# Kernel optimization log

Hardware: AMD Instinct MI355X
Metric: run time of the kernel (lower is better)

The kernel has to match this reference:

```python
import jax, jax.numpy as jnp
import numpy as np

N_NODES = 100_000
N_EDGES = 3_200_000
N_FEAT = 128
N_HID = 8
N_CLASSES = 10


def setup_inputs() -> dict:
    key = jax.random.key(0)
    ks = jax.random.split(key, 16)
    g = lambda k, shape, fan_in: jax.random.normal(k, shape, jnp.float32) / np.sqrt(fan_in)
    inp = {}
    inp['x'] = jax.random.normal(ks[0], (N_NODES, N_FEAT), jnp.float32)
    inp['edge_index'] = jax.random.randint(ks[1], (2, N_EDGES), 0, N_NODES, jnp.int32)
    # lin: Linear(F, 8)
    inp['lin_w'] = g(ks[2], (N_FEAT, N_HID), N_FEAT)
    inp['lin_b'] = jnp.zeros((N_HID,), jnp.float32)
    # conv1: GATConv(8, 8, heads=2)
    inp['w1'] = g(ks[3], (N_HID, 2 * N_HID), N_HID)
    inp['a1_src'] = g(ks[4], (2, N_HID), N_HID)
    inp['a1_dst'] = g(ks[5], (2, N_HID), N_HID)
    inp['b1'] = jnp.zeros((2 * N_HID,), jnp.float32)
    # conv2: GATConv(16, 8, heads=2)
    inp['w2'] = g(ks[6], (2 * N_HID, 2 * N_HID), 2 * N_HID)
    inp['a2_src'] = g(ks[7], (2, N_HID), N_HID)
    inp['a2_dst'] = g(ks[8], (2, N_HID), N_HID)
    inp['b2'] = jnp.zeros((2 * N_HID,), jnp.float32)
    # conv3: GATConv(16, num_classes, heads=1, concat=False)
    inp['w3'] = g(ks[9], (2 * N_HID, N_CLASSES), 2 * N_HID)
    inp['a3_src'] = g(ks[10], (1, N_CLASSES), N_CLASSES)
    inp['a3_dst'] = g(ks[11], (1, N_CLASSES), N_CLASSES)
    inp['b3'] = jnp.zeros((N_CLASSES,), jnp.float32)
    return inp


def _gat_conv(x, W, a_src, a_dst, b, src, dst, heads, out_c, concat):
    """PyG GATConv with pre-appended self-loops in (src, dst)."""
    N = x.shape[0]
    xl = (x @ W).reshape(N, heads, out_c)                 # [N,H,C]
    alpha_src = (xl * a_src[None]).sum(-1)                # [N,H]
    alpha_dst = (xl * a_dst[None]).sum(-1)                # [N,H]
    e = jax.nn.leaky_relu(alpha_src[src] + alpha_dst[dst], 0.2)  # [E,H]
    # segment softmax over destination nodes
    m = jax.ops.segment_max(e, dst, num_segments=N)
    e = jnp.exp(e - m[dst])
    s = jax.ops.segment_sum(e, dst, num_segments=N)
    alpha = e / s[dst]                                    # [E,H]
    msg = xl[src] * alpha[:, :, None]                     # [E,H,C]
    out = jax.ops.segment_sum(msg, dst, num_segments=N)   # [N,H,C]
    out = out.reshape(N, heads * out_c) if concat else out.mean(axis=1)
    return out + b


def reference(x, edge_index, lin_w, lin_b, w1, a1_src, a1_dst, b1,
              w2, a2_src, a2_dst, b2, w3, a3_src, a3_dst, b3):
    N = x.shape[0]
    loops = jnp.arange(N, dtype=edge_index.dtype)
    src = jnp.concatenate([edge_index[0], loops])
    dst = jnp.concatenate([edge_index[1], loops])
    lrelu = lambda v: jax.nn.leaky_relu(v, 0.01)
    h = lrelu(x @ lin_w + lin_b)
    h = lrelu(_gat_conv(h, w1, a1_src, a1_dst, b1, src, dst, 2, N_HID, True))
    h = lrelu(_gat_conv(h, w2, a2_src, a2_dst, b2, src, dst, 2, N_HID, True))
    h = _gat_conv(h, w3, a3_src, a3_dst, b3, src, dst, 1, N_CLASSES, False)
    return jax.nn.log_softmax(h, axis=-1)
```

## Files before the change

### kernel.cpp

```cpp
#include <hip/hip_runtime.h>
#include <hip/hip_fp16.h>
#include <math.h>

#define N_NODES 100000
#define N_EDGES 3200000
#define ET (N_EDGES + N_NODES)
#define SLOT 80
#define KMAX 5
#define SHIFT 8
#define BNODES 256
#define NBUCK 391
#define P1_T 1024
#define E_PER 8
#define P1_WG ((N_EDGES + P1_T * E_PER - 1) / (P1_T * E_PER))
#define BUILD_T 1024
#define SCAN_T 1024
#define SCAN_CHUNK 98
#define LOG2E 1.44269504088896f

typedef _Float16 h2 __attribute__((ext_vector_type(2)));

__device__ __forceinline__ float lrelu(float v, float s) { return v > 0.f ? v : v * s; }
__device__ __forceinline__ float fexp2(float x) { return __builtin_amdgcn_exp2f(x); }

__device__ __forceinline__ h2 f2h2(float f) {
    union { float f; h2 h; } u; u.f = f; return u.h;
}

__device__ __forceinline__ float fdot2(h2 a, h2 b, float c) {
#if __has_builtin(__builtin_amdgcn_fdot2)
    return __builtin_amdgcn_fdot2(a, b, c, false);
#else
    return c + (float)a.x * (float)b.x + (float)a.y * (float)b.y;
#endif
}

template <int CTRL>
__device__ __forceinline__ float dppmov(float v) {
    return __int_as_float(__builtin_amdgcn_update_dpp(0, __float_as_int(v), CTRL, 0xF, 0xF, true));
}

__device__ __forceinline__ void reduce8(float a[8], float& ssum, int lane) {
    int b0 = lane & 1, b1 = (lane >> 1) & 1, b2 = (lane >> 2) & 1;
    float q0 = (b0 ? a[4] : a[0]) + dppmov<0xB1>(b0 ? a[0] : a[4]);
    float q1 = (b0 ? a[5] : a[1]) + dppmov<0xB1>(b0 ? a[1] : a[5]);
    float q2 = (b0 ? a[6] : a[2]) + dppmov<0xB1>(b0 ? a[2] : a[6]);
    float q3 = (b0 ? a[7] : a[3]) + dppmov<0xB1>(b0 ? a[3] : a[7]);
    float r0 = (b1 ? q2 : q0) + dppmov<0x4E>(b1 ? q0 : q2);
    float r1 = (b1 ? q3 : q1) + dppmov<0x4E>(b1 ? q1 : q3);
    float t  = (b2 ? r1 : r0) + __shfl_xor(b2 ? r0 : r1, 4, 64);
    t += __shfl_xor(t, 8, 64);
    a[0] = t;
    ssum += dppmov<0xB1>(ssum);
    ssum += dppmov<0x4E>(ssum);
    ssum += __shfl_xor(ssum, 4, 64);
    ssum += __shfl_xor(ssum, 8, 64);
}

__global__ void __launch_bounds__(P1_T) part_kernel(const int* __restrict__ ei,
                                                    int* __restrict__ starts,
                                                    unsigned* __restrict__ pairs) {
    __shared__ int hist[NBUCK];
    __shared__ int scan[512];
    int t = threadIdx.x;
    for (int i = t; i < NBUCK; i += P1_T) hist[i] = 0;
    __syncthreads();
    int base = blockIdx.x * (P1_T * E_PER);
    int s[E_PER], d[E_PER], r[E_PER];
#pragma unroll
    for (int k = 0; k < E_PER; k++) {
        int e = base + k * P1_T + t;
        if (e < N_EDGES) {
            s[k] = ei[e];
            d[k] = ei[N_EDGES + e];
            r[k] = atomicAdd(&hist[d[k] >> SHIFT], 1);
        }
    }
    __syncthreads();
    if (t < 512) scan[t] = (t < NBUCK) ? hist[t] : 0;
    __syncthreads();
    for (int off = 1; off < 512; off <<= 1) {
        int v = 0, add = 0;
        if (t < 512) { v = scan[t]; if (t >= off) add = scan[t - off]; }
        __syncthreads();
        if (t < 512) scan[t] = v + add;
        __syncthreads();
    }
    if (t <= NBUCK) starts[blockIdx.x * (NBUCK + 1) + t] = base + (t ? scan[t - 1] : 0);
#pragma unroll
    for (int k = 0; k < E_PER; k++) {
        int e = base + k * P1_T + t;
        if (e < N_EDGES) {
            int b = d[k] >> SHIFT;
            int pos = (b ? scan[b - 1] : 0) + r[k];
            pairs[base + pos] = ((unsigned)(d[k] & (BNODES - 1)) << 17) | (unsigned)s[k];
        }
    }
}

__global__ void __launch_bounds__(BUILD_T) build_kernel(const int* __restrict__ starts,
                                                        const unsigned* __restrict__ pairs,
                                                        int* __restrict__ csr,
                                                        int* __restrict__ deg) {
    __shared__ int offs[BNODES];
    int b = blockIdx.x;
    int t = threadIdx.x;
    int node0 = b << SHIFT;
    if (t < BNODES) {
        int n = node0 + t;
        if (n < N_NODES) {
            csr[n * SLOT] = n;
            offs[t] = 1;
        } else offs[t] = 0;
    }
    __syncthreads();
    int wid = t >> 6, lane = t & 63;
    for (int B = wid; B < P1_WG; B += (BUILD_T / 64)) {
        int st = starts[B * (NBUCK + 1) + b];
        int en = starts[B * (NBUCK + 1) + b + 1];
        for (int i = st + lane; i < en; i += 64) {
            unsigned v = pairs[i];
            int ln = v >> 17;
            int sc = v & 0x1FFFF;
            int pos = atomicAdd(&offs[ln], 1);
            if (pos < SLOT) csr[(node0 + ln) * SLOT + pos] = sc;
        }
    }
    __syncthreads();
    if (t < BNODES) {
        int n = node0 + t;
        if (n < N_NODES) deg[n] = offs[t];
    }
}

__global__ void count_kernel(const int* __restrict__ ei, int* __restrict__ deg) {
    int e = blockIdx.x * blockDim.x + threadIdx.x;
    if (e >= ET) return;
    int d = (e < N_EDGES) ? ei[N_EDGES + e] : (e - N_EDGES);
    atomicAdd(&deg[d], 1);
}

__global__ void scan_kernel(const int* __restrict__ deg, int* __restrict__ rowptr,
                            int* __restrict__ cursor) {
    __shared__ int sums[SCAN_T];
    int t = threadIdx.x;
    int start = t * SCAN_CHUNK;
    int end = min(start + SCAN_CHUNK, N_NODES);
    int s = 0;
    for (int i = start; i < end; i++) s += deg[i];
    sums[t] = s;
    __syncthreads();
    for (int off = 1; off < SCAN_T; off <<= 1) {
        int v = sums[t];
        int add = (t >= off) ? sums[t - off] : 0;
        __syncthreads();
        sums[t] = v + add;
        __syncthreads();
    }
    int base = (t > 0) ? sums[t - 1] : 0;
    for (int i = start; i < end; i++) {
        rowptr[i] = base;
        cursor[i] = base;
        base += deg[i];
    }
    if (t == SCAN_T - 1) rowptr[N_NODES] = base;
}

__global__ void scatter_kernel(const int* __restrict__ ei, int* __restrict__ cursor,
                               int* __restrict__ csr) {
    int e = blockIdx.x * blockDim.x + threadIdx.x;
    if (e >= ET) return;
    int s, d;
    if (e < N_EDGES) { s = ei[e]; d = ei[N_EDGES + e]; } else { s = d = e - N_EDGES; }
    int pos = atomicAdd(&cursor[d], 1);
    csr[pos] = s;
}

template <int CIN, int H, int C, int XLS>
__global__ void prep_kernel(const float* __restrict__ hin, const float* __restrict__ W,
                            const float* __restrict__ a_src, const float* __restrict__ a_dst,
                            __half* __restrict__ xl, float* __restrict__ asrc,
                            float* __restrict__ adst) {
    __shared__ float Ws[CIN * H * C];
    __shared__ float As[H * C];
    __shared__ float Ad[H * C];
    for (int i = threadIdx.x; i < CIN * H * C; i += blockDim.x) Ws[i] = W[i];
    for (int i = threadIdx.x; i < H * C; i += blockDim.x) {
        As[i] = a_src[i] * LOG2E;
        Ad[i] = a_dst[i] * LOG2E;
    }
    __syncthreads();
    int n = blockIdx.x * blockDim.x + threadIdx.x;
    if (n >= N_NODES) return;
    float hreg[CIN];
#pragma unroll
    for (int i = 0; i < CIN; i += 4) {
        float4 v = *(const float4*)&hin[n * CIN + i];
        hreg[i] = v.x; hreg[i + 1] = v.y; hreg[i + 2] = v.z; hreg[i + 3] = v.w;
    }
#pragma unroll
    for (int h = 0; h < H; h++) {
        float as = 0.f, ad = 0.f;
#pragma unroll
        for (int c = 0; c < C; c++) {
            float v = 0.f;
#pragma unroll
            for (int i = 0; i < CIN; i++) v += hreg[i] * Ws[i * H * C + h * C + c];
            xl[n * XLS + h * C + c] = __float2half_rn(v);
            as += v * As[h * C + c];
            ad += v * Ad[h * C + c];
        }
        asrc[n * H + h] = as;
        adst[n * H + h] = ad;
    }
#pragma unroll
    for (int c = H * C; c < XLS; c++) xl[n * XLS + c] = __float2half_rn(0.f);
}

template <int H, int C, int XLS>
__global__ __launch_bounds__(256) void prep_lin_kernel(
        const float* __restrict__ x, const float* __restrict__ lw, const float* __restrict__ lb,
        const float* __restrict__ W, const float* __restrict__ a_src,
        const float* __restrict__ a_dst, __half* __restrict__ xl,
        float* __restrict__ asrc, float* __restrict__ adst) {
    __shared__ float LW[128 * 8];
    __shared__ float Ws[8 * H * C];
    __shared__ float As[H * C];
    __shared__ float Ad[H * C];
    __shared__ float Lb[8];
    for (int i = threadIdx.x; i < 128 * 8; i += 256) LW[i] = lw[i];
    for (int i = threadIdx.x; i < 8 * H * C; i += 256) Ws[i] = W[i];
    for (int i = threadIdx.x; i < H * C; i += 256) {
        As[i] = a_src[i] * LOG2E;
        Ad[i] = a_dst[i] * LOG2E;
    }
    if (threadIdx.x < 8) Lb[threadIdx.x] = lb[threadIdx.x];
    __syncthreads();
    int n = blockIdx.x * blockDim.x + threadIdx.x;
    if (n >= N_NODES) return;
    float hreg[8];
#pragma unroll
    for (int c = 0; c < 8; c++) hreg[c] = 0.f;
#pragma unroll 8
    for (int i = 0; i < 128; i += 4) {
        float4 v = *(const float4*)&x[n * 128 + i];
#pragma unroll
        for (int c = 0; c < 8; c++) hreg[c] += v.x * LW[(i + 0) * 8 + c];
#pragma unroll
        for (int c = 0; c < 8; c++) hreg[c] += v.y * LW[(i + 1) * 8 + c];
#pragma unroll
        for (int c = 0; c < 8; c++) hreg[c] += v.z * LW[(i + 2) * 8 + c];
#pragma unroll
        for (int c = 0; c < 8; c++) hreg[c] += v.w * LW[(i + 3) * 8 + c];
    }
#pragma unroll
    for (int c = 0; c < 8; c++) hreg[c] = lrelu(hreg[c] + Lb[c], 0.01f);
#pragma unroll
    for (int h = 0; h < H; h++) {
        float as = 0.f, ad = 0.f;
#pragma unroll
        for (int c = 0; c < C; c++) {
            float v = 0.f;
#pragma unroll
            for (int i = 0; i < 8; i++) v += hreg[i] * Ws[i * H * C + h * C + c];
            xl[n * XLS + h * C + c] = __float2half_rn(v);
            as += v * As[h * C + c];
            ad += v * Ad[h * C + c];
        }
        asrc[n * H + h] = as;
        adst[n * H + h] = ad;
    }
#pragma unroll
    for (int c = H * C; c < XLS; c++) xl[n * XLS + c] = __float2half_rn(0.f);
}

__global__ __launch_bounds__(256) void gat64_h2(const int* __restrict__ cnt_,
                                                const int* __restrict__ csr,
                                                const float* __restrict__ a_src,
                                                const float* __restrict__ adst,
                                                const __half* __restrict__ xl,
                                                const float* __restrict__ b,
                                                float* __restrict__ hout) {
    int wg = blockIdx.x * 4 + (threadIdx.x >> 6);
    int lane = threadIdx.x & 63;
    int eg = lane & 15;
    int q  = (lane >> 4) & 1;
    int nd = lane >> 5;
    int n = wg * 2 + nd;
    float4 as0 = *(const float4*)&a_src[q * 8];
    float4 as1 = *(const float4*)&a_src[q * 8 + 4];
    h2 av0 = {(_Float16)(as0.x * LOG2E), (_Float16)(as0.y * LOG2E)};
    h2 av1 = {(_Float16)(as0.z * LOG2E), (_Float16)(as0.w * LOG2E)};
    h2 av2 = {(_Float16)(as1.x * LOG2E), (_Float16)(as1.y * LOG2E)};
    h2 av3 = {(_Float16)(as1.z * LOG2E), (_Float16)(as1.w * LOG2E)};
    int cnt = min(cnt_[n], SLOT);
    float ad = adst[n * 2 + q];
    int idx[KMAX];
#pragma unroll
    for (int k = 0; k < KMAX; k++) {
        int i = eg + (k << 4);
        idx[k] = (i < cnt) ? csr[n * SLOT + i] : -1;
    }
    float ssum = 0.f;
    float a[8] = {0.f, 0.f, 0.f, 0.f, 0.f, 0.f, 0.f, 0.f};
#pragma unroll
    for (int k = 0; k < KMAX; k++) {
        int s = idx[k];
        if (s >= 0) {
            float4 raw = *(const float4*)&xl[s * 16 + q * 8];
            h2 x0 = f2h2(raw.x), x1 = f2h2(raw.y), x2 = f2h2(raw.z), x3 = f2h2(raw.w);
            float e = fdot2(x0, av0, fdot2(x1, av1, fdot2(x2, av2, fdot2(x3, av3, ad))));
            float w = fexp2(fmaxf(e, 0.2f * e));
            ssum += w;
            a[0] += w * (float)x0.x; a[1] += w * (float)x0.y;
            a[2] += w * (float)x1.x; a[3] += w * (float)x1.y;
            a[4] += w * (float)x2.x; a[5] += w * (float)x2.y;
            a[6] += w * (float)x3.x; a[7] += w * (float)x3.y;
        }
    }
    reduce8(a, ssum, lane);
    if ((lane & 8) == 0) {
        int ch = 8 * q + 4 * (lane & 1) + 2 * ((lane >> 1) & 1) + ((lane >> 2) & 1);
        hout[n * 16 + ch] = lrelu(a[0] / ssum + b[ch], 0.01f);
    }
}

__global__ __launch_bounds__(256) void gat64_ls(const int* __restrict__ cnt_,
                                                const int* __restrict__ csr,
                                                const float* __restrict__ a_src,
                                                const float* __restrict__ adst,
                                                const __half* __restrict__ xl,
                                                const float* __restrict__ b,
                                                float* __restrict__ out) {
    int wg = blockIdx.x * 4 + (threadIdx.x >> 6);
    int lane = threadIdx.x & 63;
    int eg = lane & 15;
    int q  = (lane >> 4) & 1;
    int nd = lane >> 5;
    int n = wg * 2 + nd;
    float avf[8];
#pragma unroll
    for (int j = 0; j < 8; j++) {
        int c = q * 8 + j;
        avf[j] = (c < 10) ? a_src[c] * LOG2E : 0.f;
    }
    h2 av0 = {(_Float16)avf[0], (_Float16)avf[1]};
    h2 av1 = {(_Float16)avf[2], (_Float16)avf[3]};
    h2 av2 = {(_Float16)avf[4], (_Float16)avf[5]};
    h2 av3 = {(_Float16)avf[6], (_Float16)avf[7]};
    int cnt = min(cnt_[n], SLOT);
    float adh = adst[n] * 0.5f;
    int idx[KMAX];
#pragma unroll
    for (int k = 0; k < KMAX; k++) {
        int i = eg + (k << 4);
        idx[k] = (i < cnt) ? csr[n * SLOT + i] : -1;
    }
    float ssum = 0.f;
    float a[8] = {0.f, 0.f, 0.f, 0.f, 0.f, 0.f, 0.f, 0.f};
#pragma unroll
    for (int k = 0; k < KMAX; k++) {
        int s = idx[k];
        if (s >= 0) {
            float4 raw = *(const float4*)&xl[s * 16 + q * 8];
            h2 x0 = f2h2(raw.x), x1 = f2h2(raw.y), x2 = f2h2(raw.z), x3 = f2h2(raw.w);
            float part = fdot2(x0, av0, fdot2(x1, av1, fdot2(x2, av2, fdot2(x3, av3, adh))));
            float e = part + __shfl_xor(part, 16, 64);
            float w = fexp2(fmaxf(e, 0.2f * e));
            ssum += w;
            a[0] += w * (float)x0.x; a[1] += w * (float)x0.y;
            a[2] += w * (float)x1.x; a[3] += w * (float)x1.y;
            a[4] += w * (float)x2.x; a[5] += w * (float)x2.y;
            a[6] += w * (float)x3.x; a[7] += w * (float)x3.y;
        }
    }
    reduce8(a, ssum, lane);
    int ch = 8 * q + 4 * (lane & 1) + 2 * ((lane >> 1) & 1) + ((lane >> 2) & 1);
    float u = (ch < 10) ? a[0] / ssum + b[ch] : -INFINITY;
    float m = u;
    m = fmaxf(m, dppmov<0xB1>(m));
    m = fmaxf(m, dppmov<0x4E>(m));
    m = fmaxf(m, __shfl_xor(m, 4, 64));
    m = fmaxf(m, __shfl_xor(m, 8, 64));
    m = fmaxf(m, __shfl_xor(m, 16, 64));
    float ex = (ch < 10 && (lane & 8) == 0) ? __expf(u - m) : 0.f;
    ex += dppmov<0xB1>(ex);
    ex += dppmov<0x4E>(ex);
    ex += __shfl_xor(ex, 4, 64);
    ex += __shfl_xor(ex, 8, 64);
    ex += __shfl_xor(ex, 16, 64);
    float lse = m + __logf(ex);
    if ((lane & 8) == 0 && ch < 10) out[n * 10 + ch] = u - lse;
}

__global__ void gat16_h2(const int* __restrict__ rowptr, const int* __restrict__ csr,
                         const float* __restrict__ asrc, const float* __restrict__ adst,
                         const __half* __restrict__ xl, const float* __restrict__ b,
                         float* __restrict__ hout) {
    int tid = blockIdx.x * blockDim.x + threadIdx.x;
    int wave = tid >> 6;
    int lane = threadIdx.x & 63;
    int g = lane >> 4;
    int c = lane & 15;
    int h = c >> 3;
    int n = wave * 4 + g;
    if (n >= N_NODES) return;
    int beg = rowptr[n], cnt = rowptr[n + 1] - beg;
    float adn = adst[n * 2 + h];
    float ssum = 0.f, pa = 0.f;
#pragma unroll 4
    for (int i = 0; i < cnt; i++) {
        int s = csr[beg + i];
        float e = asrc[s * 2 + h] + adn;
        float w = fexp2(fmaxf(e, 0.2f * e));
        ssum += w;
        pa += w * __half2float(xl[s * 16 + c]);
    }
    hout[n * 16 + c] = lrelu(pa / ssum + b[c], 0.01f);
}

__global__ void gat16_ls(const int* __restrict__ rowptr, const int* __restrict__ csr,
                         const float* __restrict__ asrc, const float* __restrict__ adst,
                         const __half* __restrict__ xl, const float* __restrict__ b,
                         float* __restrict__ out) {
    int tid = blockIdx.x * blockDim.x + threadIdx.x;
    int wave = tid >> 6;
    int lane = threadIdx.x & 63;
    int g = lane >> 4;
    int c = lane & 15;
    int n = wave * 4 + g;
    if (n >= N_NODES) return;
    int beg = rowptr[n], cnt = rowptr[n + 1] - beg;
    float adn = adst[n];
    float ssum = 0.f, pa = 0.f;
#pragma unroll 4
    for (int i = 0; i < cnt; i++) {
        int s = csr[beg + i];
        float e = asrc[s] + adn;
        float w = fexp2(fmaxf(e, 0.2f * e));
        ssum += w;
        pa += w * __half2float(xl[s * 16 + c]);
    }
    float v = pa / ssum + ((c < 10) ? b[c] : 0.f);
    float vm = (c < 10) ? v : -INFINITY;
#pragma unroll
    for (int off = 8; off >= 1; off >>= 1) vm = fmaxf(vm, __shfl_xor(vm, off, 16));
    float ex = (c < 10) ? __expf(v - vm) : 0.f;
    float sum = ex;
#pragma unroll
    for (int off = 8; off >= 1; off >>= 1) sum += __shfl_xor(sum, off, 16);
    float lse = vm + __logf(sum);
    if (c < 10) out[n * 10 + c] = v - lse;
}

extern "C" void kernel_launch(void* const* d_in, const int* in_sizes, int n_in,
                              void* d_out, int out_size, void* d_ws, size_t ws_size,
                              hipStream_t stream) {
    const float* x     = (const float*)d_in[0];
    const int*   ei    = (const int*)d_in[1];
    const float* lin_w = (const float*)d_in[2];
    const float* lin_b = (const float*)d_in[3];
    const float* w1    = (const float*)d_in[4];
    const float* a1s   = (const float*)d_in[5];
    const float* a1d   = (const float*)d_in[6];
    const float* b1    = (const float*)d_in[7];
    const float* w2    = (const float*)d_in[8];
    const float* a2s   = (const float*)d_in[9];
    const float* a2d   = (const float*)d_in[10];
    const float* b2    = (const float*)d_in[11];
    const float* w3    = (const float*)d_in[12];
    const float* a3s   = (const float*)d_in[13];
    const float* a3d   = (const float*)d_in[14];
    const float* b3    = (const float*)d_in[15];

    float* ws = (float*)d_ws;
    float* slotH  = ws;
    __half* slotX = (__half*)(ws + 1600000);
    float* as_    = ws + 3200000;
    float* ad_    = ws + 3400000;
    unsigned* pairs = (unsigned*)ws;
    int* csrP = (int*)(ws + 3600000);
    int* degP = csrP + (size_t)N_NODES * SLOT;
    int* startsP = degP + N_NODES;
    size_t need_new = (size_t)(3600000 + (size_t)N_NODES * SLOT + N_NODES
                               + (size_t)P1_WG * (NBUCK + 1) + 64) * 4;

    int use_bucket = (ws_size >= need_new) ? 1 : 0;

    int* degC    = (int*)(ws + 3600000);
    int* rowptrC = degC + N_NODES;
    int* cursorC = rowptrC + N_NODES + 1;
    int* csrC    = cursorC + N_NODES;

    dim3 B(256);
    int nb_n  = (N_NODES + 255) / 256;
    int nb_et = (ET + 255) / 256;
    int nb_g  = (N_NODES + 15) / 16;
    int nb_w2 = N_NODES / 8;

    if (use_bucket) {
        part_kernel<<<P1_WG, P1_T, 0, stream>>>(ei, startsP, pairs);
        build_kernel<<<NBUCK, BUILD_T, 0, stream>>>(startsP, pairs, csrP, degP);
    } else {
        hipMemsetAsync(degC, 0, N_NODES * sizeof(int), stream);
        count_kernel<<<nb_et, B, 0, stream>>>(ei, degC);
        scan_kernel<<<1, SCAN_T, 0, stream>>>(degC, rowptrC, cursorC);
        scatter_kernel<<<nb_et, B, 0, stream>>>(ei, cursorC, csrC);
    }

    prep_lin_kernel<2, 8, 16><<<nb_n, B, 0, stream>>>(x, lin_w, lin_b, w1, a1s, a1d,
                                                      slotX, as_, ad_);
    if (use_bucket) gat64_h2<<<nb_w2, B, 0, stream>>>(degP, csrP, a1s, ad_, slotX, b1, slotH);
    else            gat16_h2<<<nb_g, B, 0, stream>>>(rowptrC, csrC, as_, ad_, slotX, b1, slotH);

    prep_kernel<16, 2, 8, 16><<<nb_n, B, 0, stream>>>(slotH, w2, a2s, a2d, slotX, as_, ad_);
    if (use_bucket) gat64_h2<<<nb_w2, B, 0, stream>>>(degP, csrP, a2s, ad_, slotX, b2, slotH);
    else            gat16_h2<<<nb_g, B, 0, stream>>>(rowptrC, csrC, as_, ad_, slotX, b2, slotH);

    prep_kernel<16, 1, 10, 16><<<nb_n, B, 0, stream>>>(slotH, w3, a3s, a3d, slotX, as_, ad_);
    if (use_bucket) gat64_ls<<<nb_w2, B, 0, stream>>>(degP, csrP, a3s, ad_, slotX, b3, (float*)d_out);
    else            gat16_ls<<<nb_g, B, 0, stream>>>(rowptrC, csrC, as_, ad_, slotX, b3, (float*)d_out);
}
```

Before: 280.2 us.

## Fuse linear prep into partition kernel and next-layer prep into GAT aggregation

Result: faster. 274.0 us (-2.2%).

```diff
diff --git a/kernel.cpp b/kernel.cpp
--- a/kernel.cpp
+++ b/kernel.cpp
@@ -13,6 +13,7 @@
 #define P1_T 1024
 #define E_PER 8
 #define P1_WG ((N_EDGES + P1_T * E_PER - 1) / (P1_T * E_PER))
+#define NB_N ((N_NODES + 255) / 256)
 #define BUILD_T 1024
 #define SCAN_T 1024
 #define SCAN_CHUNK 98
@@ -57,43 +58,90 @@
     ssum += __shfl_xor(ssum, 8, 64);
 }
 
-__global__ void __launch_bounds__(P1_T) part_kernel(const int* __restrict__ ei,
-                                                    int* __restrict__ starts,
-                                                    unsigned* __restrict__ pairs) {
+__global__ void __launch_bounds__(P1_T) partlin_kernel(
+        const int* __restrict__ ei, int* __restrict__ starts, unsigned* __restrict__ pairs,
+        const float* __restrict__ x, const float* __restrict__ lw, const float* __restrict__ lb,
+        const float* __restrict__ W, const float* __restrict__ a_dst,
+        __half* __restrict__ xl, float* __restrict__ adst) {
     __shared__ int hist[NBUCK];
     __shared__ int scan[512];
+    __shared__ float LW[128 * 8];
+    __shared__ float Ws[8 * 16];
+    __shared__ float Ad[16];
+    __shared__ float Lb[8];
     int t = threadIdx.x;
-    for (int i = t; i < NBUCK; i += P1_T) hist[i] = 0;
-    __syncthreads();
-    int base = blockIdx.x * (P1_T * E_PER);
-    int s[E_PER], d[E_PER], r[E_PER];
-#pragma unroll
-    for (int k = 0; k < E_PER; k++) {
-        int e = base + k * P1_T + t;
-        if (e < N_EDGES) {
-            s[k] = ei[e];
-            d[k] = ei[N_EDGES + e];
-            r[k] = atomicAdd(&hist[d[k] >> SHIFT], 1);
-        }
-    }
-    __syncthreads();
-    if (t < 512) scan[t] = (t < NBUCK) ? hist[t] : 0;
-    __syncthreads();
-    for (int off = 1; off < 512; off <<= 1) {
-        int v = 0, add = 0;
-        if (t < 512) { v = scan[t]; if (t >= off) add = scan[t - off]; }
+    if (blockIdx.x < P1_WG) {
+        for (int i = t; i < NBUCK; i += P1_T) hist[i] = 0;
         __syncthreads();
-        if (t < 512) scan[t] = v + add;
+        int base = blockIdx.x * (P1_T * E_PER);
+        int s[E_PER], d[E_PER], r[E_PER];
+#pragma unroll
+        for (int k = 0; k < E_PER; k++) {
+            int e = base + k * P1_T + t;
+            if (e < N_EDGES) {
+                s[k] = ei[e];
+                d[k] = ei[N_EDGES + e];
+                r[k] = atomicAdd(&hist[d[k] >> SHIFT], 1);
+            }
+        }
         __syncthreads();
-    }
-    if (t <= NBUCK) starts[blockIdx.x * (NBUCK + 1) + t] = base + (t ? scan[t - 1] : 0);
-#pragma unroll
-    for (int k = 0; k < E_PER; k++) {
-        int e = base + k * P1_T + t;
-        if (e < N_EDGES) {
-            int b = d[k] >> SHIFT;
-            int pos = (b ? scan[b - 1] : 0) + r[k];
-            pairs[base + pos] = ((unsigned)(d[k] & (BNODES - 1)) << 17) | (unsigned)s[k];
+        if (t < 512) scan[t] = (t < NBUCK) ? hist[t] : 0;
+        __syncthreads();
+        for (int off = 1; off < 512; off <<= 1) {
+            int v = 0, add = 0;
+            if (t < 512) { v = scan[t]; if (t >= off) add = scan[t - off]; }
+            __syncthreads();
+            if (t < 512) scan[t] = v + add;
+            __syncthreads();
+        }
+        if (t <= NBUCK) starts[blockIdx.x * (NBUCK + 1) + t] = base + (t ? scan[t - 1] : 0);
+#pragma unroll
+        for (int k = 0; k < E_PER; k++) {
+            int e = base + k * P1_T + t;
+            if (e < N_EDGES) {
+                int b = d[k] >> SHIFT;
+                int pos = (b ? scan[b - 1] : 0) + r[k];
+                pairs[base + pos] = ((unsigned)(d[k] & (BNODES - 1)) << 17) | (unsigned)s[k];
+            }
+        }
+    } else {
+        for (int i = t; i < 128 * 8; i += P1_T) LW[i] = lw[i];
+        for (int i = t; i < 8 * 16; i += P1_T) Ws[i] = W[i];
+        for (int i = t; i < 16; i += P1_T) Ad[i] = a_dst[i] * LOG2E;
+        if (t < 8) Lb[t] = lb[t];
+        __syncthreads();
+        if (t >= 256) return;
+        int n = (blockIdx.x - P1_WG) * 256 + t;
+        if (n >= N_NODES) return;
+        float hreg[8];
+#pragma unroll
+        for (int c = 0; c < 8; c++) hreg[c] = 0.f;
+#pragma unroll 8
+        for (int i = 0; i < 128; i += 4) {
+            float4 v = *(const float4*)&x[n * 128 + i];
+#pragma unroll
+            for (int c = 0; c < 8; c++) hreg[c] += v.x * LW[(i + 0) * 8 + c];
+#pragma unroll
+            for (int c = 0; c < 8; c++) hreg[c] += v.y * LW[(i + 1) * 8 + c];
+#pragma unroll
+            for (int c = 0; c < 8; c++) hreg[c] += v.z * LW[(i + 2) * 8 + c];
+#pragma unroll
+            for (int c = 0; c < 8; c++) hreg[c] += v.w * LW[(i + 3) * 8 + c];
+        }
+#pragma unroll
+        for (int c = 0; c < 8; c++) hreg[c] = lrelu(hreg[c] + Lb[c], 0.01f);
+#pragma unroll
+        for (int h = 0; h < 2; h++) {
+            float ad = 0.f;
+#pragma unroll
+            for (int c = 0; c < 8; c++) {
+                float v = 0.f;
+#pragma unroll
+                for (int i = 0; i < 8; i++) v += hreg[i] * Ws[i * 16 + h * 8 + c];
+                xl[n * 16 + h * 8 + c] = __float2half_rn(v);
+                ad += v * Ad[h * 8 + c];
+            }
+            adst[n * 2 + h] = ad;
         }
     }
 }
@@ -274,14 +322,22 @@
     for (int c = H * C; c < XLS; c++) xl[n * XLS + c] = __float2half_rn(0.f);
 }
 
-__global__ __launch_bounds__(256) void gat64_h2(const int* __restrict__ cnt_,
-                                                const int* __restrict__ csr,
-                                                const float* __restrict__ a_src,
-                                                const float* __restrict__ adst,
-                                                const __half* __restrict__ xl,
-                                                const float* __restrict__ b,
-                                                float* __restrict__ hout) {
-    int wg = blockIdx.x * 4 + (threadIdx.x >> 6);
+template <int CN, int HN>
+__global__ __launch_bounds__(256) void gat64_h2_fused(
+        const int* __restrict__ cnt_, const int* __restrict__ csr,
+        const float* __restrict__ a_src, const float* __restrict__ adst,
+        const __half* __restrict__ xl, const float* __restrict__ b,
+        const float* __restrict__ Wn_g, const float* __restrict__ adn_g,
+        __half* __restrict__ xl_next, float* __restrict__ adst_next) {
+    __shared__ float hsm[8][16];
+    __shared__ float vsm[8][16];
+    __shared__ float Wn[16 * CN];
+    __shared__ float Adn[CN];
+    for (int i = threadIdx.x; i < 16 * CN; i += 256) Wn[i] = Wn_g[i];
+    for (int i = threadIdx.x; i < CN; i += 256) Adn[i] = adn_g[i] * LOG2E;
+
+    int wid = threadIdx.x >> 6;
+    int wg = blockIdx.x * 4 + wid;
     int lane = threadIdx.x & 63;
     int eg = lane & 15;
     int q  = (lane >> 4) & 1;
@@ -321,7 +377,28 @@
     reduce8(a, ssum, lane);
     if ((lane & 8) == 0) {
         int ch = 8 * q + 4 * (lane & 1) + 2 * ((lane >> 1) & 1) + ((lane >> 2) & 1);
-        hout[n * 16 + ch] = lrelu(a[0] / ssum + b[ch], 0.01f);
+        hsm[(wid << 1) | nd][ch] = lrelu(a[0] / ssum + b[ch], 0.01f);
+    }
+    __syncthreads();
+    if (threadIdx.x < 128) {
+        int ln = threadIdx.x >> 4, c = threadIdx.x & 15;
+        float v = 0.f;
+        if (c < CN) {
+#pragma unroll
+            for (int i = 0; i < 16; i++) v += hsm[ln][i] * Wn[i * CN + c];
+        }
+        int n2 = blockIdx.x * 8 + ln;
+        xl_next[n2 * 16 + c] = __float2half_rn(v);
+        vsm[ln][c] = v;
+    }
+    __syncthreads();
+    if (threadIdx.x < 8 * HN) {
+        int ln = threadIdx.x / HN, h = threadIdx.x % HN;
+        const int CH = CN / HN;
+        float adn = 0.f;
+#pragma unroll
+        for (int j = 0; j < CH; j++) adn += vsm[ln][h * CH + j] * Adn[h * CH + j];
+        adst_next[(blockIdx.x * 8 + ln) * HN + h] = adn;
     }
 }
 
@@ -478,12 +555,12 @@
     __half* slotX = (__half*)(ws + 1600000);
     float* as_    = ws + 3200000;
     float* ad_    = ws + 3400000;
-    unsigned* pairs = (unsigned*)ws;
     int* csrP = (int*)(ws + 3600000);
     int* degP = csrP + (size_t)N_NODES * SLOT;
     int* startsP = degP + N_NODES;
+    unsigned* pairs = (unsigned*)(startsP + (size_t)P1_WG * (NBUCK + 1));
     size_t need_new = (size_t)(3600000 + (size_t)N_NODES * SLOT + N_NODES
-                               + (size_t)P1_WG * (NBUCK + 1) + 64) * 4;
+                               + (size_t)P1_WG * (NBUCK + 1) + N_EDGES + 64) * 4;
 
     int use_bucket = (ws_size >= need_new) ? 1 : 0;
 
@@ -493,31 +570,38 @@
     int* csrC    = cursorC + N_NODES;
 
     dim3 B(256);
-    int nb_n  = (N_NODES + 255) / 256;
+    int nb_n  = NB_N;
     int nb_et = (ET + 255) / 256;
     int nb_g  = (N_NODES + 15) / 16;
     int nb_w2 = N_NODES / 8;
 
     if (use_bucket) {
-        part_kernel<<<P1_WG, P1_T, 0, stream>>>(ei, startsP, pairs);
+        __half* xl1 = slotX;
+        __half* xl2 = (__half*)slotH;
+        __half* xl3 = slotX;
+        float* ad1 = ad_;
+        float* ad2 = as_;
+        float* ad3 = ad_;
+        partlin_kernel<<<P1_WG + NB_N, P1_T, 0, stream>>>(ei, startsP, pairs,
+                                                          x, lin_w, lin_b, w1, a1d, xl1, ad1);
         build_kernel<<<NBUCK, BUILD_T, 0, stream>>>(startsP, pairs, csrP, degP);
+        gat64_h2_fused<16, 2><<<nb_w2, B, 0, stream>>>(degP, csrP, a1s, ad1, xl1, b1,
+                                                       w2, a2d, xl2, ad2);
+        gat64_h2_fused<10, 1><<<nb_w2, B, 0, stream>>>(degP, csrP, a2s, ad2, xl2, b2,
+                                                       w3, a3d, xl3, ad3);
+        gat64_ls<<<nb_w2, B, 0, stream>>>(degP, csrP, a3s, ad3, xl3, b3, (float*)d_out);
     } else {
         hipMemsetAsync(degC, 0, N_NODES * sizeof(int), stream);
         count_kernel<<<nb_et, B, 0, stream>>>(ei, degC);
         scan_kernel<<<1, SCAN_T, 0, stream>>>(degC, rowptrC, cursorC);
         scatter_kernel<<<nb_et, B, 0, stream>>>(ei, cursorC, csrC);
-    }
-
-    prep_lin_kernel<2, 8, 16><<<nb_n, B, 0, stream>>>(x, lin_w, lin_b, w1, a1s, a1d,
-                                                      slotX, as_, ad_);
-    if (use_bucket) gat64_h2<<<nb_w2, B, 0, stream>>>(degP, csrP, a1s, ad_, slotX, b1, slotH);
-    else            gat16_h2<<<nb_g, B, 0, stream>>>(rowptrC, csrC, as_, ad_, slotX, b1, slotH);
-
-    prep_kernel<16, 2, 8, 16><<<nb_n, B, 0, stream>>>(slotH, w2, a2s, a2d, slotX, as_, ad_);
-    if (use_bucket) gat64_h2<<<nb_w2, B, 0, stream>>>(degP, csrP, a2s, ad_, slotX, b2, slotH);
-    else            gat16_h2<<<nb_g, B, 0, stream>>>(rowptrC, csrC, as_, ad_, slotX, b2, slotH);
-
-    prep_kernel<16, 1, 10, 16><<<nb_n, B, 0, stream>>>(slotH, w3, a3s, a3d, slotX, as_, ad_);
-    if (use_bucket) gat64_ls<<<nb_w2, B, 0, stream>>>(degP, csrP, a3s, ad_, slotX, b3, (float*)d_out);
-    else            gat16_ls<<<nb_g, B, 0, stream>>>(rowptrC, csrC, as_, ad_, slotX, b3, (float*)d_out);
-}
+
+        prep_lin_kernel<2, 8, 16><<<nb_n, B, 0, stream>>>(x, lin_w, lin_b, w1, a1s, a1d,
+                                                          slotX, as_, ad_);
+        gat16_h2<<<nb_g, B, 0, stream>>>(rowptrC, csrC, as_, ad_, slotX, b1, slotH);
+        prep_kernel<16, 2, 8, 16><<<nb_n, B, 0, stream>>>(slotH, w2, a2s, a2d, slotX, as_, ad_);
+        gat16_h2<<<nb_g, B, 0, stream>>>(rowptrC, csrC, as_, ad_, slotX, b2, slotH);
+        prep_kernel<16, 1, 10, 16><<<nb_n, B, 0, stream>>>(slotH, w3, a3s, a3d, slotX, as_, ad_);
+        gat16_ls<<<nb_g, B, 0, stream>>>(rowptrC, csrC, as_, ad_, slotX, b3, (float*)d_out);
+    }
+}
```
